# Performance work log

Measured on AMD Instinct MI355X. Metric: run time of the kernel, lower is better.

Reference implementation:

```python
import jax, jax.numpy as jnp
import numpy as np

C_Z = 128
C_HID = 128
EPS = 1e-5


def _layer_norm(x, w, b):
    mu = jnp.mean(x, axis=-1, keepdims=True)
    var = jnp.var(x, axis=-1, keepdims=True)
    return (x - mu) * jax.lax.rsqrt(var + EPS) * w + b


def setup_inputs() -> dict:
    key = jax.random.key(0)
    ks = jax.random.split(key, 10)
    B, S = 1, 512
    s_in = 1.0 / np.sqrt(C_Z)
    s_hid = 1.0 / np.sqrt(C_HID)
    return {
        "z": jax.random.normal(ks[0], (B, S, S, C_Z), dtype=jnp.float32),
        "ln_w": jnp.ones((C_Z,), jnp.float32),
        "ln_b": jnp.zeros((C_Z,), jnp.float32),
        "Wa": jax.random.uniform(ks[1], (C_Z, C_HID), jnp.float32, -s_in, s_in),
        "ba": jax.random.uniform(ks[2], (C_HID,), jnp.float32, -s_in, s_in),
        "Wb": jax.random.uniform(ks[3], (C_Z, C_HID), jnp.float32, -s_in, s_in),
        "bb": jax.random.uniform(ks[4], (C_HID,), jnp.float32, -s_in, s_in),
        "Wg": jax.random.uniform(ks[5], (C_Z, C_Z), jnp.float32, -s_in, s_in),
        "bg": jax.random.uniform(ks[6], (C_Z,), jnp.float32, -s_in, s_in),
        "lno_w": jnp.ones((C_HID,), jnp.float32),
        "lno_b": jnp.zeros((C_HID,), jnp.float32),
        "Wout": jax.random.uniform(ks[7], (C_HID, C_Z), jnp.float32, -s_hid, s_hid),
        "bout": jax.random.uniform(ks[8], (C_Z,), jnp.float32, -s_hid, s_hid),
    }


def reference(z, ln_w, ln_b, Wa, ba, Wb, bb, Wg, bg, lno_w, lno_b, Wout, bout):
    # z: [B, S, S, c_z]
    z = _layer_norm(z, ln_w, ln_b)
    a = jnp.einsum('bikz,zc->bikc', z, Wa) + ba  # [B,S,S,c_hid]
    b = jnp.einsum('bjkz,zc->bjkc', z, Wb) + bb
    # outgoing: contract shared index k -> c_hidden independent SxS matmuls
    ab = jnp.einsum('bikc,bjkc->bijc', a, b)
    ab = _layer_norm(ab, lno_w, lno_b)
    ab = jnp.einsum('bijc,cz->bijz', ab, Wout) + bout
    g = jax.nn.sigmoid(jnp.einsum('bijz,zy->bijy', z, Wg) + bg)
    return g * ab
```

## Files before the change

kernel.cpp:

```cpp
#include <hip/hip_runtime.h>
#include <cstdint>

#define S5 512
#define PLANE ((size_t)S5 * S5)

typedef __attribute__((ext_vector_type(4))) float f32x4;
typedef __attribute__((ext_vector_type(8))) short bf16x8;

__device__ __forceinline__ unsigned short f2bf(float f) {
  union { float f; unsigned u; } v; v.f = f;
  unsigned r = v.u + 0x7fffu + ((v.u >> 16) & 1u);
  return (unsigned short)(r >> 16);
}
__device__ __forceinline__ unsigned pack2(float a, float b) {
  return (unsigned)f2bf(a) | ((unsigned)f2bf(b) << 16);
}
__device__ __forceinline__ float bf2f(unsigned short h) {
  union { unsigned u; float f; } v; v.u = ((unsigned)h) << 16;
  return v.f;
}

__global__ void k0_prep(const float* __restrict__ Wa, const float* __restrict__ Wb,
                        const float* __restrict__ Wg, const float* __restrict__ Wout,
                        unsigned short* __restrict__ wTab, unsigned short* __restrict__ wgT,
                        unsigned short* __restrict__ woutT) {
  int t = blockIdx.x * 256 + threadIdx.x;
  if (t < 32768) {
    int cg = t >> 7, zz = t & 127;
    const float* W = (cg < 128) ? Wa : Wb;
    int c = cg & 127;
    wTab[t] = f2bf(W[zz * 128 + c]);
  } else if (t < 49152) {
    int u = t - 32768; int y = u >> 7, zz = u & 127;
    wgT[u] = f2bf(Wg[zz * 128 + y]);
  } else if (t < 65536) {
    int u = t - 49152; int zo = u >> 7, c = u & 127;
    woutT[u] = f2bf(Wout[c * 128 + zo]);
  }
}

__launch_bounds__(256, 2)
__global__ void k1_ln_proj(const float* __restrict__ z,
                           const float* __restrict__ ln_w, const float* __restrict__ ln_b,
                           const float* __restrict__ ba, const float* __restrict__ bb,
                           const unsigned short* __restrict__ wTab,
                           unsigned short* __restrict__ aT, unsigned short* __restrict__ bT) {
  __shared__ unsigned short zs[64][136];
  __shared__ float lnw[128], lnb[128];
  int t = threadIdx.x;
  int lane = t & 63, w = t >> 6;
  int row0 = blockIdx.x * 64;

  if (t < 128) lnw[t] = ln_w[t];
  else lnb[t - 128] = ln_b[t - 128];

  bf16x8 wf[4][4];
#pragma unroll
  for (int tt = 0; tt < 4; ++tt) {
    int gct = w * 4 + tt;
    int wr = gct * 16 + (lane & 15);
#pragma unroll
    for (int kk = 0; kk < 4; ++kk)
      wf[tt][kk] = *reinterpret_cast<const bf16x8*>(wTab + wr * 128 + kk * 32 + ((lane >> 4) << 3));
  }
  __syncthreads();

  {
    int r = t >> 2, q = t & 3;
    const float* zp = z + (size_t)(row0 + r) * 128 + q * 32;
    float v[32]; float s = 0.f, s2 = 0.f;
#pragma unroll
    for (int i = 0; i < 8; ++i) {
      f32x4 x = *reinterpret_cast<const f32x4*>(zp + i * 4);
      v[i * 4] = x[0]; v[i * 4 + 1] = x[1]; v[i * 4 + 2] = x[2]; v[i * 4 + 3] = x[3];
      s  += x[0] + x[1] + x[2] + x[3];
      s2 += x[0] * x[0] + x[1] * x[1] + x[2] * x[2] + x[3] * x[3];
    }
    s  += __shfl_xor(s, 1);  s  += __shfl_xor(s, 2);
    s2 += __shfl_xor(s2, 1); s2 += __shfl_xor(s2, 2);
    float mu = s * (1.f / 128.f);
    float var = s2 * (1.f / 128.f) - mu * mu;
    float rstd = rsqrtf(var + 1e-5f);
    unsigned pk[16];
#pragma unroll
    for (int i = 0; i < 16; ++i) {
      int c = q * 32 + i * 2;
      float a0 = (v[i * 2] - mu) * rstd * lnw[c] + lnb[c];
      float a1 = (v[i * 2 + 1] - mu) * rstd * lnw[c + 1] + lnb[c + 1];
      pk[i] = pack2(a0, a1);
    }
#pragma unroll
    for (int i = 0; i < 4; ++i)
      *reinterpret_cast<uint4*>(&zs[r][q * 32 + i * 8]) =
          make_uint4(pk[i * 4], pk[i * 4 + 1], pk[i * 4 + 2], pk[i * 4 + 3]);
  }
  __syncthreads();

  f32x4 acc[4][4];
#pragma unroll
  for (int a = 0; a < 4; ++a)
#pragma unroll
    for (int b2 = 0; b2 < 4; ++b2) { f32x4 zv = {0.f, 0.f, 0.f, 0.f}; acc[a][b2] = zv; }

#pragma unroll
  for (int kk = 0; kk < 4; ++kk) {
    bf16x8 af[4];
#pragma unroll
    for (int rt = 0; rt < 4; ++rt)
      af[rt] = *reinterpret_cast<const bf16x8*>(&zs[rt * 16 + (lane & 15)][kk * 32 + ((lane >> 4) << 3)]);
#pragma unroll
    for (int rt = 0; rt < 4; ++rt)
#pragma unroll
      for (int tt = 0; tt < 4; ++tt)
        acc[rt][tt] = __builtin_amdgcn_mfma_f32_16x16x32_bf16(af[rt], wf[tt][kk], acc[rt][tt], 0, 0, 0);
  }

#pragma unroll
  for (int tt = 0; tt < 4; ++tt) {
    int gct = w * 4 + tt;
    int m = gct >> 3;
    int c = ((gct & 7) << 4) + (lane & 15);
    float bias = (m ? bb : ba)[c];
    unsigned short* plane = (m ? bT : aT) + (size_t)c * PLANE;
#pragma unroll
    for (int rt = 0; rt < 4; ++rt) {
      int ik = row0 + rt * 16 + ((lane >> 4) << 2);
      f32x4 v = acc[rt][tt];
      uint2 st = make_uint2(pack2(v[0] + bias, v[1] + bias), pack2(v[2] + bias, v[3] + bias));
      *reinterpret_cast<uint2*>(plane + ik) = st;
    }
  }
}

__launch_bounds__(256, 2)
__global__ void k2_gemm(const unsigned short* __restrict__ aT,
                        const unsigned short* __restrict__ bT,
                        unsigned short* __restrict__ abT) {
  __shared__ unsigned short As[128][72];
  __shared__ unsigned short Bs[128][72];
  int t = threadIdx.x, lane = t & 63, w = t >> 6;
  int c = blockIdx.x >> 4;
  int tid = blockIdx.x & 15;
  int i0 = (tid >> 2) * 128, j0 = (tid & 3) * 128;
  const unsigned short* Ap = aT + (size_t)c * PLANE;
  const unsigned short* Bp = bT + (size_t)c * PLANE;
  int rw = (w >> 1) * 64, cw = (w & 1) * 64;

  f32x4 acc[4][4];
#pragma unroll
  for (int a = 0; a < 4; ++a)
#pragma unroll
    for (int b2 = 0; b2 < 4; ++b2) { f32x4 zv = {0.f, 0.f, 0.f, 0.f}; acc[a][b2] = zv; }

  int sr = t >> 3;
  int sc = (t & 7) * 8;
  for (int k0 = 0; k0 < 512; k0 += 64) {
#pragma unroll
    for (int p = 0; p < 4; ++p) {
      int r = p * 32 + sr;
      *reinterpret_cast<uint4*>(&As[r][sc]) =
          *reinterpret_cast<const uint4*>(Ap + (size_t)(i0 + r) * 512 + k0 + sc);
      *reinterpret_cast<uint4*>(&Bs[r][sc]) =
          *reinterpret_cast<const uint4*>(Bp + (size_t)(j0 + r) * 512 + k0 + sc);
    }
    __syncthreads();
#pragma unroll
    for (int kk = 0; kk < 2; ++kk) {
      bf16x8 af[4], bfr[4];
#pragma unroll
      for (int rt = 0; rt < 4; ++rt)
        af[rt] = *reinterpret_cast<const bf16x8*>(&As[rw + rt * 16 + (lane & 15)][kk * 32 + ((lane >> 4) << 3)]);
#pragma unroll
      for (int ct = 0; ct < 4; ++ct)
        bfr[ct] = *reinterpret_cast<const bf16x8*>(&Bs[cw + ct * 16 + (lane & 15)][kk * 32 + ((lane >> 4) << 3)]);
#pragma unroll
      for (int rt = 0; rt < 4; ++rt)
#pragma unroll
        for (int ct = 0; ct < 4; ++ct)
          acc[rt][ct] = __builtin_amdgcn_mfma_f32_16x16x32_bf16(af[rt], bfr[ct], acc[rt][ct], 0, 0, 0);
    }
    __syncthreads();
  }

  unsigned short* Op = abT + (size_t)c * PLANE;
#pragma unroll
  for (int rt = 0; rt < 4; ++rt)
#pragma unroll
    for (int ct = 0; ct < 4; ++ct) {
      int j = j0 + cw + ct * 16 + (lane & 15);
      int ib = i0 + rw + rt * 16 + ((lane >> 4) << 2);
      f32x4 v = acc[rt][ct];
#pragma unroll
      for (int rr = 0; rr < 4; ++rr)
        Op[(size_t)(ib + rr) * 512 + j] = f2bf(v[rr]);
    }
}

__launch_bounds__(256, 2)
__global__ void k3_final(const float* __restrict__ z,
                         const unsigned short* __restrict__ abT,
                         const unsigned short* __restrict__ wgT,
                         const unsigned short* __restrict__ woutT,
                         const float* __restrict__ ln_w, const float* __restrict__ ln_b,
                         const float* __restrict__ lno_w, const float* __restrict__ lno_b,
                         const float* __restrict__ bg, const float* __restrict__ bout,
                         float* __restrict__ out) {
  __shared__ unsigned short Xab[64][136];
  __shared__ unsigned short Xz[64][136];
  __shared__ unsigned short wS[128][136];
  __shared__ float cvec[6 * 128];
  int t = threadIdx.x, lane = t & 63, w = t >> 6;
  int i0 = (blockIdx.x >> 4) * 2;
  int j0 = (blockIdx.x & 15) * 32;

  for (int i = t; i < 768; i += 256) {
    int which = i >> 7, idx = i & 127; float vv;
    if      (which == 0) vv = ln_w[idx];
    else if (which == 1) vv = ln_b[idx];
    else if (which == 2) vv = lno_w[idx];
    else if (which == 3) vv = lno_b[idx];
    else if (which == 4) vv = bg[idx];
    else                 vv = bout[idx];
    cvec[i] = vv;
  }
  __syncthreads();

  {
    int p = t >> 2, q = t & 3;
    int li = p >> 5, jj = p & 31;
    size_t grow = (size_t)(i0 + li) * 512 + (j0 + jj);
    const float* zp = z + grow * 128 + q * 32;
    float v[32]; float s = 0.f, s2 = 0.f;
#pragma unroll
    for (int i = 0; i < 8; ++i) {
      f32x4 x = *reinterpret_cast<const f32x4*>(zp + i * 4);
      v[i * 4] = x[0]; v[i * 4 + 1] = x[1]; v[i * 4 + 2] = x[2]; v[i * 4 + 3] = x[3];
      s  += x[0] + x[1] + x[2] + x[3];
      s2 += x[0] * x[0] + x[1] * x[1] + x[2] * x[2] + x[3] * x[3];
    }
    s  += __shfl_xor(s, 1);  s  += __shfl_xor(s, 2);
    s2 += __shfl_xor(s2, 1); s2 += __shfl_xor(s2, 2);
    float mu = s * (1.f / 128.f);
    float var = s2 * (1.f / 128.f) - mu * mu;
    float rstd = rsqrtf(var + 1e-5f);
    unsigned pk[16];
#pragma unroll
    for (int i = 0; i < 16; ++i) {
      int cc = q * 32 + i * 2;
      pk[i] = pack2((v[i * 2] - mu) * rstd * cvec[cc] + cvec[128 + cc],
                    (v[i * 2 + 1] - mu) * rstd * cvec[cc + 1] + cvec[128 + cc + 1]);
    }
#pragma unroll
    for (int i = 0; i < 4; ++i)
      *reinterpret_cast<uint4*>(&Xz[p][q * 32 + i * 8]) =
          make_uint4(pk[i * 4], pk[i * 4 + 1], pk[i * 4 + 2], pk[i * 4 + 3]);
  }

  {
    int c = t >> 1, li = t & 1;
    const unsigned short* src = abT + (size_t)c * PLANE + (size_t)(i0 + li) * 512 + j0;
#pragma unroll
    for (int s4 = 0; s4 < 4; ++s4) {
      uint4 dv = *reinterpret_cast<const uint4*>(src + s4 * 8);
      unsigned uu[4] = {dv.x, dv.y, dv.z, dv.w};
#pragma unroll
      for (int e = 0; e < 4; ++e) {
        Xab[li * 32 + s4 * 8 + e * 2    ][c] = (unsigned short)(uu[e] & 0xffffu);
        Xab[li * 32 + s4 * 8 + e * 2 + 1][c] = (unsigned short)(uu[e] >> 16);
      }
    }
  }

  {
    int r = t >> 1, h = (t & 1) * 64;
#pragma unroll
    for (int s4 = 0; s4 < 8; ++s4)
      *reinterpret_cast<uint4*>(&wS[r][h + s4 * 8]) =
          *reinterpret_cast<const uint4*>(wgT + r * 128 + h + s4 * 8);
  }
  __syncthreads();

  {
    int p = t >> 2, q = t & 3;
    float v[32]; float s = 0.f, s2 = 0.f;
#pragma unroll
    for (int i4 = 0; i4 < 4; ++i4) {
      uint4 dv = *reinterpret_cast<const uint4*>(&Xab[p][q * 32 + i4 * 8]);
      unsigned uu[4] = {dv.x, dv.y, dv.z, dv.w};
#pragma unroll
      for (int e = 0; e < 4; ++e) {
        float x0 = bf2f((unsigned short)(uu[e] & 0xffffu));
        float x1 = bf2f((unsigned short)(uu[e] >> 16));
        v[i4 * 8 + e * 2] = x0; v[i4 * 8 + e * 2 + 1] = x1;
        s += x0 + x1; s2 += x0 * x0 + x1 * x1;
      }
    }
    s  += __shfl_xor(s, 1);  s  += __shfl_xor(s, 2);
    s2 += __shfl_xor(s2, 1); s2 += __shfl_xor(s2, 2);
    float mu = s * (1.f / 128.f);
    float var = s2 * (1.f / 128.f) - mu * mu;
    float rstd = rsqrtf(var + 1e-5f);
    unsigned pk[16];
#pragma unroll
    for (int i = 0; i < 16; ++i) {
      int cc = q * 32 + i * 2;
      pk[i] = pack2((v[i * 2] - mu) * rstd * cvec[256 + cc] + cvec[384 + cc],
                    (v[i * 2 + 1] - mu) * rstd * cvec[256 + cc + 1] + cvec[384 + cc + 1]);
    }
#pragma unroll
    for (int i4 = 0; i4 < 4; ++i4)
      *reinterpret_cast<uint4*>(&Xab[p][q * 32 + i4 * 8]) =
          make_uint4(pk[i4 * 4], pk[i4 * 4 + 1], pk[i4 * 4 + 2], pk[i4 * 4 + 3]);
  }
  __syncthreads();

  f32x4 ga[8];
#pragma unroll
  for (int i = 0; i < 8; ++i) { f32x4 zv = {0.f, 0.f, 0.f, 0.f}; ga[i] = zv; }
#pragma unroll
  for (int kk = 0; kk < 4; ++kk) {
    bf16x8 af = *reinterpret_cast<const bf16x8*>(&Xz[w * 16 + (lane & 15)][kk * 32 + ((lane >> 4) << 3)]);
#pragma unroll
    for (int ct = 0; ct < 8; ++ct) {
      bf16x8 bfr = *reinterpret_cast<const bf16x8*>(&wS[ct * 16 + (lane & 15)][kk * 32 + ((lane >> 4) << 3)]);
      ga[ct] = __builtin_amdgcn_mfma_f32_16x16x32_bf16(af, bfr, ga[ct], 0, 0, 0);
    }
  }
  unsigned gp[8][2];
#pragma unroll
  for (int ct = 0; ct < 8; ++ct) {
    int y = ct * 16 + (lane & 15);
    float b4 = cvec[512 + y];
    float g0 = 1.f / (1.f + expf(-(ga[ct][0] + b4)));
    float g1 = 1.f / (1.f + expf(-(ga[ct][1] + b4)));
    float g2 = 1.f / (1.f + expf(-(ga[ct][2] + b4)));
    float g3 = 1.f / (1.f + expf(-(ga[ct][3] + b4)));
    gp[ct][0] = pack2(g0, g1);
    gp[ct][1] = pack2(g2, g3);
  }
  __syncthreads();

  {
    int r = t >> 1, h = (t & 1) * 64;
#pragma unroll
    for (int s4 = 0; s4 < 8; ++s4)
      *reinterpret_cast<uint4*>(&wS[r][h + s4 * 8]) =
          *reinterpret_cast<const uint4*>(woutT + r * 128 + h + s4 * 8);
  }
  __syncthreads();

  f32x4 oa[8];
#pragma unroll
  for (int i = 0; i < 8; ++i) { f32x4 zv = {0.f, 0.f, 0.f, 0.f}; oa[i] = zv; }
#pragma unroll
  for (int kk = 0; kk < 4; ++kk) {
    bf16x8 af = *reinterpret_cast<const bf16x8*>(&Xab[w * 16 + (lane & 15)][kk * 32 + ((lane >> 4) << 3)]);
#pragma unroll
    for (int ct = 0; ct < 8; ++ct) {
      bf16x8 bfr = *reinterpret_cast<const bf16x8*>(&wS[ct * 16 + (lane & 15)][kk * 32 + ((lane >> 4) << 3)]);
      oa[ct] = __builtin_amdgcn_mfma_f32_16x16x32_bf16(af, bfr, oa[ct], 0, 0, 0);
    }
  }

#pragma unroll
  for (int ct = 0; ct < 8; ++ct) {
    int zc = ct * 16 + (lane & 15);
    float bo = cvec[640 + zc];
#pragma unroll
    for (int rr = 0; rr < 4; ++rr) {
      int p = w * 16 + ((lane >> 4) << 2) + rr;
      int li = p >> 5, jj = p & 31;
      size_t grow = (size_t)(i0 + li) * 512 + (j0 + jj);
      float gv = bf2f((unsigned short)(gp[ct][rr >> 1] >> ((rr & 1) * 16)));
      out[grow * 128 + zc] = gv * (oa[ct][rr] + bo);
    }
  }
}

extern "C" void kernel_launch(void* const* d_in, const int* in_sizes, int n_in,
                              void* d_out, int out_size, void* d_ws, size_t ws_size,
                              hipStream_t stream) {
  const float* z     = (const float*)d_in[0];
  const float* ln_w  = (const float*)d_in[1];
  const float* ln_b  = (const float*)d_in[2];
  const float* Wa    = (const float*)d_in[3];
  const float* ba    = (const float*)d_in[4];
  const float* Wb    = (const float*)d_in[5];
  const float* bb    = (const float*)d_in[6];
  const float* Wg    = (const float*)d_in[7];
  const float* bg    = (const float*)d_in[8];
  const float* lno_w = (const float*)d_in[9];
  const float* lno_b = (const float*)d_in[10];
  const float* Wout  = (const float*)d_in[11];
  const float* bout  = (const float*)d_in[12];
  float* out = (float*)d_out;

  char* ws = (char*)d_ws;
  unsigned short* aT    = (unsigned short*)(ws);
  unsigned short* bT    = (unsigned short*)(ws + 67108864);
  unsigned short* abT   = (unsigned short*)(ws + 134217728);
  unsigned short* wTab  = (unsigned short*)(ws + 201326592);
  unsigned short* wgT   = (unsigned short*)(ws + 201392128);
  unsigned short* woutT = (unsigned short*)(ws + 201424896);

  k0_prep<<<256, 256, 0, stream>>>(Wa, Wb, Wg, Wout, wTab, wgT, woutT);
  k1_ln_proj<<<4096, 256, 0, stream>>>(z, ln_w, ln_b, ba, bb, wTab, aT, bT);
  k2_gemm<<<2048, 256, 0, stream>>>(aT, bT, abT);
  k3_final<<<4096, 256, 0, stream>>>(z, abT, wgT, woutT, ln_w, ln_b, lno_w, lno_b,
                                     bg, bout, out);
}
```

Measured before the change: 465.4 us.

## Restructure final kernel with register-resident LN, split-bf16 MFMA and LDS-transposed stores

The final kernel is rewritten so each wave keeps its layernormed z and ab rows in registers as hi/lo bf16 pairs and feeds them straight to MFMA, with weights read from global memory instead of being staged in LDS. The ab tile is staged through a swizzled LDS buffer. The projection kernel now transposes its output through LDS so each thread writes contiguous 128-bit rows to the planes. The GEMM kernel remaps block IDs to interleave channels across the grid. The split-bf16 trick doubles the MFMA count in the final kernel to gain accuracy, and direct global weight reads may raise cache traffic.

Measured after the change: 590.7 us. 1.27x slower.

```diff
diff --git a/kernel.cpp b/kernel.cpp
--- a/kernel.cpp
+++ b/kernel.cpp
@@ -18,6 +18,12 @@
 __device__ __forceinline__ float bf2f(unsigned short h) {
   union { unsigned u; float f; } v; v.u = ((unsigned)h) << 16;
   return v.f;
+}
+__device__ __forceinline__ void pack2hl(float a, float b, unsigned& hi, unsigned& lo) {
+  unsigned short ah = f2bf(a), bh = f2bf(b);
+  unsigned short al = f2bf(a - bf2f(ah)), bl = f2bf(b - bf2f(bh));
+  hi = (unsigned)ah | ((unsigned)bh << 16);
+  lo = (unsigned)al | ((unsigned)bl << 16);
 }
 
 __global__ void k0_prep(const float* __restrict__ Wa, const float* __restrict__ Wb,
@@ -46,6 +52,7 @@
                            const unsigned short* __restrict__ wTab,
                            unsigned short* __restrict__ aT, unsigned short* __restrict__ bT) {
   __shared__ unsigned short zs[64][136];
+  __shared__ unsigned obuf[32][257];
   __shared__ float lnw[128], lnb[128];
   int t = threadIdx.x;
   int lane = t & 63, w = t >> 6;
@@ -118,17 +125,30 @@
 #pragma unroll
   for (int tt = 0; tt < 4; ++tt) {
     int gct = w * 4 + tt;
+    int oc = gct * 16 + (lane & 15);
     int m = gct >> 3;
-    int c = ((gct & 7) << 4) + (lane & 15);
+    int c = oc & 127;
     float bias = (m ? bb : ba)[c];
-    unsigned short* plane = (m ? bT : aT) + (size_t)c * PLANE;
 #pragma unroll
     for (int rt = 0; rt < 4; ++rt) {
-      int ik = row0 + rt * 16 + ((lane >> 4) << 2);
+      int q = rt * 8 + ((lane >> 4) << 1);
       f32x4 v = acc[rt][tt];
-      uint2 st = make_uint2(pack2(v[0] + bias, v[1] + bias), pack2(v[2] + bias, v[3] + bias));
-      *reinterpret_cast<uint2*>(plane + ik) = st;
-    }
+      obuf[q][oc]     = pack2(v[0] + bias, v[1] + bias);
+      obuf[q + 1][oc] = pack2(v[2] + bias, v[3] + bias);
+    }
+  }
+  __syncthreads();
+
+  {
+    int m = t >> 7, c = t & 127;
+    unsigned short* plane = (m ? bT : aT) + (size_t)c * PLANE + row0;
+    unsigned r[32];
+#pragma unroll
+    for (int q = 0; q < 32; ++q) r[q] = obuf[q][t];
+#pragma unroll
+    for (int u = 0; u < 8; ++u)
+      *reinterpret_cast<uint4*>(plane + u * 8) =
+          make_uint4(r[u * 4], r[u * 4 + 1], r[u * 4 + 2], r[u * 4 + 3]);
   }
 }
 
@@ -139,8 +159,9 @@
   __shared__ unsigned short As[128][72];
   __shared__ unsigned short Bs[128][72];
   int t = threadIdx.x, lane = t & 63, w = t >> 6;
-  int c = blockIdx.x >> 4;
-  int tid = blockIdx.x & 15;
+  int bid = ((blockIdx.x & 7) << 8) | (blockIdx.x >> 3);
+  int c = bid >> 4;
+  int tid = bid & 15;
   int i0 = (tid >> 2) * 128, j0 = (tid & 3) * 128;
   const unsigned short* Ap = aT + (size_t)c * PLANE;
   const unsigned short* Bp = bT + (size_t)c * PLANE;
@@ -205,174 +226,160 @@
                          const float* __restrict__ lno_w, const float* __restrict__ lno_b,
                          const float* __restrict__ bg, const float* __restrict__ bout,
                          float* __restrict__ out) {
-  __shared__ unsigned short Xab[64][136];
-  __shared__ unsigned short Xz[64][136];
-  __shared__ unsigned short wS[128][136];
-  __shared__ float cvec[6 * 128];
+  __shared__ unsigned XabU[64][64];
   int t = threadIdx.x, lane = t & 63, w = t >> 6;
-  int i0 = (blockIdx.x >> 4) * 2;
-  int j0 = (blockIdx.x & 15) * 32;
-
-  for (int i = t; i < 768; i += 256) {
-    int which = i >> 7, idx = i & 127; float vv;
-    if      (which == 0) vv = ln_w[idx];
-    else if (which == 1) vv = ln_b[idx];
-    else if (which == 2) vv = lno_w[idx];
-    else if (which == 3) vv = lno_b[idx];
-    else if (which == 4) vv = bg[idx];
-    else                 vv = bout[idx];
-    cvec[i] = vv;
-  }
-  __syncthreads();
+  int i = blockIdx.x >> 3;
+  int j0 = (blockIdx.x & 7) * 64;
 
   {
-    int p = t >> 2, q = t & 3;
-    int li = p >> 5, jj = p & 31;
-    size_t grow = (size_t)(i0 + li) * 512 + (j0 + jj);
-    const float* zp = z + grow * 128 + q * 32;
-    float v[32]; float s = 0.f, s2 = 0.f;
-#pragma unroll
-    for (int i = 0; i < 8; ++i) {
-      f32x4 x = *reinterpret_cast<const f32x4*>(zp + i * 4);
-      v[i * 4] = x[0]; v[i * 4 + 1] = x[1]; v[i * 4 + 2] = x[2]; v[i * 4 + 3] = x[3];
-      s  += x[0] + x[1] + x[2] + x[3];
-      s2 += x[0] * x[0] + x[1] * x[1] + x[2] * x[2] + x[3] * x[3];
-    }
-    s  += __shfl_xor(s, 1);  s  += __shfl_xor(s, 2);
-    s2 += __shfl_xor(s2, 1); s2 += __shfl_xor(s2, 2);
+    int c2 = lane;
+    int p0 = w * 16;
+    const unsigned short* sA = abT + (size_t)(2 * c2) * PLANE + (size_t)i * 512 + j0 + p0;
+    const unsigned short* sB = sA + PLANE;
+    unsigned short la[16], lb[16];
+    *reinterpret_cast<uint4*>(la)     = *reinterpret_cast<const uint4*>(sA);
+    *reinterpret_cast<uint4*>(la + 8) = *reinterpret_cast<const uint4*>(sA + 8);
+    *reinterpret_cast<uint4*>(lb)     = *reinterpret_cast<const uint4*>(sB);
+    *reinterpret_cast<uint4*>(lb + 8) = *reinterpret_cast<const uint4*>(sB + 8);
+#pragma unroll
+    for (int k = 0; k < 16; ++k) {
+      int p = p0 + k;
+      int col = ((((c2 >> 2) ^ (p & 7)) & 15) << 2) | (c2 & 3);
+      XabU[p][col] = (unsigned)la[k] | ((unsigned)lb[k] << 16);
+    }
+  }
+
+  int ks = lane >> 4;
+  int prow16 = lane & 15;
+  int jpos = j0 + w * 16 + prow16;
+  size_t growA = (size_t)i * 512 + jpos;
+
+  bf16x8 pzh[4], pzl[4];
+  {
+    const float* zp = z + growA * 128;
+    float x[4][8]; float s = 0.f, s2 = 0.f;
+#pragma unroll
+    for (int kk = 0; kk < 4; ++kk) {
+      int cb = ks * 8 + kk * 32;
+      f32x4 a0 = *reinterpret_cast<const f32x4*>(zp + cb);
+      f32x4 a1 = *reinterpret_cast<const f32x4*>(zp + cb + 4);
+#pragma unroll
+      for (int e = 0; e < 4; ++e) { x[kk][e] = a0[e]; x[kk][4 + e] = a1[e]; }
+      s  += a0[0] + a0[1] + a0[2] + a0[3] + a1[0] + a1[1] + a1[2] + a1[3];
+      s2 += a0[0]*a0[0] + a0[1]*a0[1] + a0[2]*a0[2] + a0[3]*a0[3]
+          + a1[0]*a1[0] + a1[1]*a1[1] + a1[2]*a1[2] + a1[3]*a1[3];
+    }
+    s  += __shfl_xor(s, 16);  s  += __shfl_xor(s, 32);
+    s2 += __shfl_xor(s2, 16); s2 += __shfl_xor(s2, 32);
     float mu = s * (1.f / 128.f);
     float var = s2 * (1.f / 128.f) - mu * mu;
     float rstd = rsqrtf(var + 1e-5f);
-    unsigned pk[16];
-#pragma unroll
-    for (int i = 0; i < 16; ++i) {
-      int cc = q * 32 + i * 2;
-      pk[i] = pack2((v[i * 2] - mu) * rstd * cvec[cc] + cvec[128 + cc],
-                    (v[i * 2 + 1] - mu) * rstd * cvec[cc + 1] + cvec[128 + cc + 1]);
-    }
-#pragma unroll
-    for (int i = 0; i < 4; ++i)
-      *reinterpret_cast<uint4*>(&Xz[p][q * 32 + i * 8]) =
-          make_uint4(pk[i * 4], pk[i * 4 + 1], pk[i * 4 + 2], pk[i * 4 + 3]);
-  }
-
+#pragma unroll
+    for (int kk = 0; kk < 4; ++kk) {
+      int cb = ks * 8 + kk * 32;
+      f32x4 w0 = *reinterpret_cast<const f32x4*>(ln_w + cb);
+      f32x4 w1 = *reinterpret_cast<const f32x4*>(ln_w + cb + 4);
+      f32x4 b0 = *reinterpret_cast<const f32x4*>(ln_b + cb);
+      f32x4 b1 = *reinterpret_cast<const f32x4*>(ln_b + cb + 4);
+      float y0 = (x[kk][0]-mu)*rstd*w0[0]+b0[0], y1 = (x[kk][1]-mu)*rstd*w0[1]+b0[1];
+      float y2 = (x[kk][2]-mu)*rstd*w0[2]+b0[2], y3 = (x[kk][3]-mu)*rstd*w0[3]+b0[3];
+      float y4 = (x[kk][4]-mu)*rstd*w1[0]+b1[0], y5 = (x[kk][5]-mu)*rstd*w1[1]+b1[1];
+      float y6 = (x[kk][6]-mu)*rstd*w1[2]+b1[2], y7 = (x[kk][7]-mu)*rstd*w1[3]+b1[3];
+      union { unsigned u[4]; bf16x8 v; } H, L;
+      pack2hl(y0, y1, H.u[0], L.u[0]);
+      pack2hl(y2, y3, H.u[1], L.u[1]);
+      pack2hl(y4, y5, H.u[2], L.u[2]);
+      pack2hl(y6, y7, H.u[3], L.u[3]);
+      pzh[kk] = H.v; pzl[kk] = L.v;
+    }
+  }
+
+  f32x4 ga[8];
+#pragma unroll
+  for (int q = 0; q < 8; ++q) { f32x4 zv = {0.f, 0.f, 0.f, 0.f}; ga[q] = zv; }
+#pragma unroll
+  for (int kk = 0; kk < 4; ++kk) {
+    int cb = ks * 8 + kk * 32;
+#pragma unroll
+    for (int ct = 0; ct < 8; ++ct) {
+      bf16x8 bfr = *reinterpret_cast<const bf16x8*>(wgT + (ct * 16 + prow16) * 128 + cb);
+      ga[ct] = __builtin_amdgcn_mfma_f32_16x16x32_bf16(pzh[kk], bfr, ga[ct], 0, 0, 0);
+      ga[ct] = __builtin_amdgcn_mfma_f32_16x16x32_bf16(pzl[kk], bfr, ga[ct], 0, 0, 0);
+    }
+  }
+#pragma unroll
+  for (int ct = 0; ct < 8; ++ct) {
+    float b4 = bg[ct * 16 + prow16];
+#pragma unroll
+    for (int rr = 0; rr < 4; ++rr)
+      ga[ct][rr] = 1.f / (1.f + expf(-(ga[ct][rr] + b4)));
+  }
+
+  __syncthreads();
+
+  bf16x8 pah[4], pal[4];
   {
-    int c = t >> 1, li = t & 1;
-    const unsigned short* src = abT + (size_t)c * PLANE + (size_t)(i0 + li) * 512 + j0;
-#pragma unroll
-    for (int s4 = 0; s4 < 4; ++s4) {
-      uint4 dv = *reinterpret_cast<const uint4*>(src + s4 * 8);
-      unsigned uu[4] = {dv.x, dv.y, dv.z, dv.w};
-#pragma unroll
-      for (int e = 0; e < 4; ++e) {
-        Xab[li * 32 + s4 * 8 + e * 2    ][c] = (unsigned short)(uu[e] & 0xffffu);
-        Xab[li * 32 + s4 * 8 + e * 2 + 1][c] = (unsigned short)(uu[e] >> 16);
+    int p = w * 16 + prow16;
+    const unsigned* row = &XabU[p][0];
+    float x[4][8]; float s = 0.f, s2 = 0.f;
+#pragma unroll
+    for (int kk = 0; kk < 4; ++kk) {
+      int chunk = ((ks + 4 * kk) ^ (p & 7)) & 15;
+      bf16x8 raw = *reinterpret_cast<const bf16x8*>(row + (chunk << 2));
+#pragma unroll
+      for (int e = 0; e < 8; ++e) {
+        float f = bf2f((unsigned short)raw[e]);
+        x[kk][e] = f; s += f; s2 += f * f;
       }
     }
-  }
-
-  {
-    int r = t >> 1, h = (t & 1) * 64;
-#pragma unroll
-    for (int s4 = 0; s4 < 8; ++s4)
-      *reinterpret_cast<uint4*>(&wS[r][h + s4 * 8]) =
-          *reinterpret_cast<const uint4*>(wgT + r * 128 + h + s4 * 8);
-  }
-  __syncthreads();
-
-  {
-    int p = t >> 2, q = t & 3;
-    float v[32]; float s = 0.f, s2 = 0.f;
-#pragma unroll
-    for (int i4 = 0; i4 < 4; ++i4) {
-      uint4 dv = *reinterpret_cast<const uint4*>(&Xab[p][q * 32 + i4 * 8]);
-      unsigned uu[4] = {dv.x, dv.y, dv.z, dv.w};
-#pragma unroll
-      for (int e = 0; e < 4; ++e) {
-        float x0 = bf2f((unsigned short)(uu[e] & 0xffffu));
-        float x1 = bf2f((unsigned short)(uu[e] >> 16));
-        v[i4 * 8 + e * 2] = x0; v[i4 * 8 + e * 2 + 1] = x1;
-        s += x0 + x1; s2 += x0 * x0 + x1 * x1;
-      }
-    }
-    s  += __shfl_xor(s, 1);  s  += __shfl_xor(s, 2);
-    s2 += __shfl_xor(s2, 1); s2 += __shfl_xor(s2, 2);
+    s  += __shfl_xor(s, 16);  s  += __shfl_xor(s, 32);
+    s2 += __shfl_xor(s2, 16); s2 += __shfl_xor(s2, 32);
     float mu = s * (1.f / 128.f);
     float var = s2 * (1.f / 128.f) - mu * mu;
     float rstd = rsqrtf(var + 1e-5f);
-    unsigned pk[16];
-#pragma unroll
-    for (int i = 0; i < 16; ++i) {
-      int cc = q * 32 + i * 2;
-      pk[i] = pack2((v[i * 2] - mu) * rstd * cvec[256 + cc] + cvec[384 + cc],
-                    (v[i * 2 + 1] - mu) * rstd * cvec[256 + cc + 1] + cvec[384 + cc + 1]);
-    }
-#pragma unroll
-    for (int i4 = 0; i4 < 4; ++i4)
-      *reinterpret_cast<uint4*>(&Xab[p][q * 32 + i4 * 8]) =
-          make_uint4(pk[i4 * 4], pk[i4 * 4 + 1], pk[i4 * 4 + 2], pk[i4 * 4 + 3]);
-  }
-  __syncthreads();
-
-  f32x4 ga[8];
-#pragma unroll
-  for (int i = 0; i < 8; ++i) { f32x4 zv = {0.f, 0.f, 0.f, 0.f}; ga[i] = zv; }
+#pragma unroll
+    for (int kk = 0; kk < 4; ++kk) {
+      int cb = ks * 8 + kk * 32;
+      f32x4 w0 = *reinterpret_cast<const f32x4*>(lno_w + cb);
+      f32x4 w1 = *reinterpret_cast<const f32x4*>(lno_w + cb + 4);
+      f32x4 b0 = *reinterpret_cast<const f32x4*>(lno_b + cb);
+      f32x4 b1 = *reinterpret_cast<const f32x4*>(lno_b + cb + 4);
+      float y0 = (x[kk][0]-mu)*rstd*w0[0]+b0[0], y1 = (x[kk][1]-mu)*rstd*w0[1]+b0[1];
+      float y2 = (x[kk][2]-mu)*rstd*w0[2]+b0[2], y3 = (x[kk][3]-mu)*rstd*w0[3]+b0[3];
+      float y4 = (x[kk][4]-mu)*rstd*w1[0]+b1[0], y5 = (x[kk][5]-mu)*rstd*w1[1]+b1[1];
+      float y6 = (x[kk][6]-mu)*rstd*w1[2]+b1[2], y7 = (x[kk][7]-mu)*rstd*w1[3]+b1[3];
+      union { unsigned u[4]; bf16x8 v; } H, L;
+      pack2hl(y0, y1, H.u[0], L.u[0]);
+      pack2hl(y2, y3, H.u[1], L.u[1]);
+      pack2hl(y4, y5, H.u[2], L.u[2]);
+      pack2hl(y6, y7, H.u[3], L.u[3]);
+      pah[kk] = H.v; pal[kk] = L.v;
+    }
+  }
+
+  f32x4 oa[8];
+#pragma unroll
+  for (int q = 0; q < 8; ++q) { f32x4 zv = {0.f, 0.f, 0.f, 0.f}; oa[q] = zv; }
 #pragma unroll
   for (int kk = 0; kk < 4; ++kk) {
-    bf16x8 af = *reinterpret_cast<const bf16x8*>(&Xz[w * 16 + (lane & 15)][kk * 32 + ((lane >> 4) << 3)]);
+    int cb = ks * 8 + kk * 32;
 #pragma unroll
     for (int ct = 0; ct < 8; ++ct) {
-      bf16x8 bfr = *reinterpret_cast<const bf16x8*>(&wS[ct * 16 + (lane & 15)][kk * 32 + ((lane >> 4) << 3)]);
-      ga[ct] = __builtin_amdgcn_mfma_f32_16x16x32_bf16(af, bfr, ga[ct], 0, 0, 0);
-    }
-  }
-  unsigned gp[8][2];
+      bf16x8 bfr = *reinterpret_cast<const bf16x8*>(woutT + (ct * 16 + prow16) * 128 + cb);
+      oa[ct] = __builtin_amdgcn_mfma_f32_16x16x32_bf16(pah[kk], bfr, oa[ct], 0, 0, 0);
+      oa[ct] = __builtin_amdgcn_mfma_f32_16x16x32_bf16(pal[kk], bfr, oa[ct], 0, 0, 0);
+    }
+  }
+
 #pragma unroll
   for (int ct = 0; ct < 8; ++ct) {
-    int y = ct * 16 + (lane & 15);
-    float b4 = cvec[512 + y];
-    float g0 = 1.f / (1.f + expf(-(ga[ct][0] + b4)));
-    float g1 = 1.f / (1.f + expf(-(ga[ct][1] + b4)));
-    float g2 = 1.f / (1.f + expf(-(ga[ct][2] + b4)));
-    float g3 = 1.f / (1.f + expf(-(ga[ct][3] + b4)));
-    gp[ct][0] = pack2(g0, g1);
-    gp[ct][1] = pack2(g2, g3);
-  }
-  __syncthreads();
-
-  {
-    int r = t >> 1, h = (t & 1) * 64;
-#pragma unroll
-    for (int s4 = 0; s4 < 8; ++s4)
-      *reinterpret_cast<uint4*>(&wS[r][h + s4 * 8]) =
-          *reinterpret_cast<const uint4*>(woutT + r * 128 + h + s4 * 8);
-  }
-  __syncthreads();
-
-  f32x4 oa[8];
-#pragma unroll
-  for (int i = 0; i < 8; ++i) { f32x4 zv = {0.f, 0.f, 0.f, 0.f}; oa[i] = zv; }
-#pragma unroll
-  for (int kk = 0; kk < 4; ++kk) {
-    bf16x8 af = *reinterpret_cast<const bf16x8*>(&Xab[w * 16 + (lane & 15)][kk * 32 + ((lane >> 4) << 3)]);
-#pragma unroll
-    for (int ct = 0; ct < 8; ++ct) {
-      bf16x8 bfr = *reinterpret_cast<const bf16x8*>(&wS[ct * 16 + (lane & 15)][kk * 32 + ((lane >> 4) << 3)]);
-      oa[ct] = __builtin_amdgcn_mfma_f32_16x16x32_bf16(af, bfr, oa[ct], 0, 0, 0);
-    }
-  }
-
-#pragma unroll
-  for (int ct = 0; ct < 8; ++ct) {
-    int zc = ct * 16 + (lane & 15);
-    float bo = cvec[640 + zc];
+    int zc = ct * 16 + prow16;
+    float bo = bout[zc];
 #pragma unroll
     for (int rr = 0; rr < 4; ++rr) {
-      int p = w * 16 + ((lane >> 4) << 2) + rr;
-      int li = p >> 5, jj = p & 31;
-      size_t grow = (size_t)(i0 + li) * 512 + (j0 + jj);
-      float gv = bf2f((unsigned short)(gp[ct][rr >> 1] >> ((rr & 1) * 16)));
-      out[grow * 128 + zc] = gv * (oa[ct][rr] + bo);
+      int prow = ks * 4 + rr;
+      size_t o = ((size_t)i * 512 + j0 + w * 16 + prow) * 128 + zc;
+      out[o] = ga[ct][rr] * (oa[ct][rr] + bo);
     }
   }
 }
```
